# Optimization experiments

Hardware: AMD Instinct MI355X
Metric: run time of the kernel (lower is better)

The kernel has to match this reference:

```python
import jax, jax.numpy as jnp
import numpy as np

EMBED_DIM = 512
NUM_HEADS = 8
HEAD_DIM = EMBED_DIM // NUM_HEADS
N = 4096
E = 131072
EPS = 1e-5
NEG = -1e9


def layer_norm(x, g, b):
    mu = jnp.mean(x, axis=-1, keepdims=True)
    var = jnp.mean(jnp.square(x - mu), axis=-1, keepdims=True)
    return (x - mu) * jax.lax.rsqrt(var + EPS) * g + b


def setup_inputs() -> dict:
    key = jax.random.key(0)
    ks = jax.random.split(key, 12)
    D = EMBED_DIM
    s = 1.0 / np.sqrt(D)
    return {
        "x": jax.random.normal(ks[0], (N, D), jnp.float32),
        "edge_index": jax.random.randint(ks[1], (2, E), 0, N, jnp.int64),
        "edge_weight": jax.random.uniform(ks[2], (E,), jnp.float32),
        "Wqkv": jax.random.normal(ks[3], (3 * D, D), jnp.float32) * s,
        "bqkv": jnp.zeros((3 * D,), jnp.float32),
        "Wo": jax.random.normal(ks[4], (D, D), jnp.float32) * s,
        "bo": jnp.zeros((D,), jnp.float32),
        "W1": jax.random.normal(ks[5], (D, D), jnp.float32) * s,
        "b1": jnp.zeros((D,), jnp.float32),
        "g1": jnp.ones((D,), jnp.float32),
        "beta1": jnp.zeros((D,), jnp.float32),
        "g2": jnp.ones((D,), jnp.float32),
        "beta2": jnp.zeros((D,), jnp.float32),
    }


def reference(x, edge_index, edge_weight, Wqkv, bqkv, Wo, bo, W1, b1, g1, beta1, g2, beta2):
    n = x.shape[0]
    # dense NxN additive bias: -1e9 everywhere, 0 on diagonal, edge weights at (dst, src)
    src, dst = edge_index[0], edge_index[1]
    diag = jnp.arange(n)
    bias = jnp.full((n, n), NEG, dtype=x.dtype)
    bias = bias.at[diag, diag].set(0.0)
    bias = bias.at[dst, src].set(edge_weight.astype(x.dtype))

    # multi-head self-attention (torch nn.MultiheadAttention semantics)
    qkv = x @ Wqkv.T + bqkv                       # (N, 3D)
    q, k, v = jnp.split(qkv, 3, axis=-1)          # each (N, D)
    q = q.reshape(n, NUM_HEADS, HEAD_DIM).transpose(1, 0, 2)  # (H, N, hd)
    k = k.reshape(n, NUM_HEADS, HEAD_DIM).transpose(1, 0, 2)
    v = v.reshape(n, NUM_HEADS, HEAD_DIM).transpose(1, 0, 2)
    scores = jnp.einsum("hnd,hmd->hnm", q, k) / np.sqrt(HEAD_DIM)  # (H, N, N)
    scores = scores + bias[None, :, :]
    attn = jax.nn.softmax(scores, axis=-1)
    out = jnp.einsum("hnm,hmd->hnd", attn, v)     # (H, N, hd)
    out = out.transpose(1, 0, 2).reshape(n, EMBED_DIM)
    attn_out = out @ Wo.T + bo

    # residual + LN + FFN (single linear, no activation) + residual + LN
    h = layer_norm(x + attn_out, g1, beta1)
    h = layer_norm(h + (h @ W1.T + b1), g2, beta2)
    return h
```

## Files before the change

### kernel.cpp

```cpp
#include <hip/hip_runtime.h>

#define NNODES 4096
#define DIM 512
#define QKVD 1536
#define MAXE 96

typedef __bf16 bf16_t;
typedef bf16_t bf16x8 __attribute__((ext_vector_type(8)));
typedef bf16_t bf16x2 __attribute__((ext_vector_type(2)));
typedef float f32x4 __attribute__((ext_vector_type(4)));
typedef unsigned int uint;

__global__ __launch_bounds__(256) void cast_all_k(const float* __restrict__ x,
                                                  const float* __restrict__ wqkv,
                                                  const float* __restrict__ wo,
                                                  const float* __restrict__ w1,
                                                  bf16_t* __restrict__ xb,
                                                  bf16_t* __restrict__ wqkvb,
                                                  bf16_t* __restrict__ wob,
                                                  bf16_t* __restrict__ w1b,
                                                  uint* __restrict__ deg) {
  int i = blockIdx.x * 256 + threadIdx.x;
  if (blockIdx.x < 16) deg[i] = 0u;
  const float* src;
  bf16_t* dst;
  int off;
  if (i < 524288) { src = x; dst = xb; off = i; }
  else if (i < 720896) { src = wqkv; dst = wqkvb; off = i - 524288; }
  else if (i < 786432) { src = wo; dst = wob; off = i - 720896; }
  else { src = w1; dst = w1b; off = i - 786432; }
  float4 v = ((const float4*)src)[off];
  dst[4 * off + 0] = (bf16_t)v.x;
  dst[4 * off + 1] = (bf16_t)v.y;
  dst[4 * off + 2] = (bf16_t)v.z;
  dst[4 * off + 3] = (bf16_t)v.w;
}

__global__ __launch_bounds__(256) void qkv_fill_k(const bf16_t* __restrict__ A,
                                                  const bf16_t* __restrict__ B,
                                                  const float* __restrict__ bias,
                                                  bf16_t* __restrict__ Cout,
                                                  const int* __restrict__ ei,
                                                  uint* __restrict__ deg,
                                                  int* __restrict__ colv,
                                                  uint* __restrict__ eidv, int E) {
  __shared__ bf16_t As[128][40];
  __shared__ bf16_t Bs[128][40];
  const int bid = blockIdx.x;
  const int t = threadIdx.x;

  if (bid >= 384) {
    int e = (bid - 384) * 256 + t;
    if (e < E) {
      int src = ei[e] & (NNODES - 1);
      int dst = ei[E + e] & (NNODES - 1);
      uint pos = atomicAdd(&deg[dst], 1u);
      if (pos < MAXE) {
        colv[dst * MAXE + pos] = src;
        eidv[dst * MAXE + pos] = (uint)e + 1u;
      }
    }
    return;
  }

  const int lane = t & 63, w = t >> 6;
  const int wr = (w >> 1) * 64, wc = (w & 1) * 64;
  const int m0 = (bid / 12) * 128, n0 = (bid % 12) * 128;
  f32x4 acc[4][4] = {};
  const int r_ld = t >> 2;
  const int c_ld = (t & 3) * 8;

  for (int k0 = 0; k0 < 512; k0 += 32) {
#pragma unroll
    for (int seg = 0; seg < 2; ++seg) {
      int row = r_ld + seg * 64;
      *(int4*)&As[row][c_ld] = *(const int4*)(A + (long)(m0 + row) * 512 + k0 + c_ld);
      *(int4*)&Bs[row][c_ld] = *(const int4*)(B + (long)(n0 + row) * 512 + k0 + c_ld);
    }
    __syncthreads();
    bf16x8 af[4], bfr[4];
    const int kg = (lane >> 4) * 8;
#pragma unroll
    for (int i = 0; i < 4; ++i) {
      af[i] = *(const bf16x8*)&As[wr + i * 16 + (lane & 15)][kg];
      bfr[i] = *(const bf16x8*)&Bs[wc + i * 16 + (lane & 15)][kg];
    }
#pragma unroll
    for (int i = 0; i < 4; ++i)
#pragma unroll
      for (int j = 0; j < 4; ++j)
        acc[i][j] = __builtin_amdgcn_mfma_f32_16x16x32_bf16(af[i], bfr[j], acc[i][j], 0, 0, 0);
    __syncthreads();
  }

  const int cr = (lane >> 4) * 4;
  const int cc = lane & 15;
#pragma unroll
  for (int i = 0; i < 4; ++i) {
#pragma unroll
    for (int j = 0; j < 4; ++j) {
      int n = n0 + wc + j * 16 + cc;
      float bv = bias[n];
#pragma unroll
      for (int r = 0; r < 4; ++r) {
        int m = m0 + wr + i * 16 + cr + r;
        Cout[(long)m * QKVD + n] = (bf16_t)(acc[i][j][r] + bv);
      }
    }
  }
}

template <bool OUT_BF16>
__global__ __launch_bounds__(256) void gemm_bt(const bf16_t* __restrict__ A,
                                               const bf16_t* __restrict__ B,
                                               const float* __restrict__ bias,
                                               void* __restrict__ Cout,
                                               int M, int Nt, int K) {
  __shared__ bf16_t As[128][40];
  __shared__ bf16_t Bs[64][40];
  const int t = threadIdx.x;
  const int lane = t & 63, w = t >> 6;
  const int wr = (w >> 1) * 64, wc = (w & 1) * 32;
  const int m0 = blockIdx.y * 128, n0 = blockIdx.x * 64;
  f32x4 acc[4][2] = {};
  const int r_ld = t >> 2;
  const int c_ld = (t & 3) * 8;

  for (int k0 = 0; k0 < K; k0 += 32) {
    *(int4*)&As[r_ld][c_ld] = *(const int4*)(A + (long)(m0 + r_ld) * K + k0 + c_ld);
    *(int4*)&As[r_ld + 64][c_ld] = *(const int4*)(A + (long)(m0 + r_ld + 64) * K + k0 + c_ld);
    *(int4*)&Bs[r_ld][c_ld] = *(const int4*)(B + (long)(n0 + r_ld) * K + k0 + c_ld);
    __syncthreads();
    bf16x8 af[4], bfr[2];
    const int kg = (lane >> 4) * 8;
#pragma unroll
    for (int i = 0; i < 4; ++i)
      af[i] = *(const bf16x8*)&As[wr + i * 16 + (lane & 15)][kg];
#pragma unroll
    for (int j = 0; j < 2; ++j)
      bfr[j] = *(const bf16x8*)&Bs[wc + j * 16 + (lane & 15)][kg];
#pragma unroll
    for (int i = 0; i < 4; ++i)
#pragma unroll
      for (int j = 0; j < 2; ++j)
        acc[i][j] = __builtin_amdgcn_mfma_f32_16x16x32_bf16(af[i], bfr[j], acc[i][j], 0, 0, 0);
    __syncthreads();
  }

  const int cr = (lane >> 4) * 4;
  const int cc = lane & 15;
#pragma unroll
  for (int i = 0; i < 4; ++i) {
#pragma unroll
    for (int j = 0; j < 2; ++j) {
      int n = n0 + wc + j * 16 + cc;
      float bv = bias[n];
#pragma unroll
      for (int r = 0; r < 4; ++r) {
        int m = m0 + wr + i * 16 + cr + r;
        float vv = acc[i][j][r] + bv;
        if (OUT_BF16)
          ((bf16_t*)Cout)[(long)m * Nt + n] = (bf16_t)vv;
        else
          ((float*)Cout)[(long)m * Nt + n] = vv;
      }
    }
  }
}

__global__ __launch_bounds__(256) void attn_fused_k(const bf16_t* __restrict__ qkv,
                                                    const float* __restrict__ ew,
                                                    const uint* __restrict__ deg,
                                                    const int* __restrict__ colv,
                                                    const uint* __restrict__ eidv,
                                                    bf16_t* __restrict__ outb) {
  __shared__ float scs[8][MAXE + 1];
  __shared__ int srcs[MAXE + 1];
  __shared__ uint eids[MAXE + 1];
  __shared__ int vld[MAXE + 1];
  __shared__ float invs_s[8];
  __shared__ float vacc[4][DIM];

  const int i = blockIdx.x;
  const int t = threadIdx.x;
  const int lane = t & 63, w = t >> 6;

  uint dg = deg[i];
  int L = (dg < (uint)MAXE) ? (int)dg : MAXE;
  int n = L + 1;

  if (t < L) {
    srcs[t] = colv[i * MAXE + t];
    eids[t] = eidv[i * MAXE + t];
  }
  if (t == L) { srcs[L] = i; eids[L] = 0u; }
  __syncthreads();

  if (t < n) {
    int sj = srcs[t];
    uint my = eids[t];
    int ok = 1;
    for (int j = 0; j < n; ++j)
      ok &= !((srcs[j] == sj) & (eids[j] > my));
    vld[t] = ok;
  }
  __syncthreads();

  const bf16x8 qv = *(const bf16x8*)(qkv + (long)i * QKVD + lane * 8);
  {
    int e = w;
    for (; e + 4 < n; e += 8) {
      int sa = srcs[e], sb = srcs[e + 4];
      const bf16x8 ka = *(const bf16x8*)(qkv + (long)sa * QKVD + DIM + lane * 8);
      const bf16x8 kb = *(const bf16x8*)(qkv + (long)sb * QKVD + DIM + lane * 8);
      float s0 = 0.f, s1 = 0.f;
#pragma unroll
      for (int j = 0; j < 8; ++j) {
        s0 += (float)qv[j] * (float)ka[j];
        s1 += (float)qv[j] * (float)kb[j];
      }
      s0 += __shfl_xor(s0, 1); s1 += __shfl_xor(s1, 1);
      s0 += __shfl_xor(s0, 2); s1 += __shfl_xor(s1, 2);
      s0 += __shfl_xor(s0, 4); s1 += __shfl_xor(s1, 4);
      if ((lane & 7) == 0) {
        int h = lane >> 3;
        float b0 = (eids[e] == 0u) ? 0.f : ew[eids[e] - 1u];
        float b1 = (eids[e + 4] == 0u) ? 0.f : ew[eids[e + 4] - 1u];
        scs[h][e] = vld[e] ? (s0 * 0.125f + b0) : -1e30f;
        scs[h][e + 4] = vld[e + 4] ? (s1 * 0.125f + b1) : -1e30f;
      }
    }
    if (e < n) {
      int sa = srcs[e];
      const bf16x8 ka = *(const bf16x8*)(qkv + (long)sa * QKVD + DIM + lane * 8);
      float s0 = 0.f;
#pragma unroll
      for (int j = 0; j < 8; ++j) s0 += (float)qv[j] * (float)ka[j];
      s0 += __shfl_xor(s0, 1);
      s0 += __shfl_xor(s0, 2);
      s0 += __shfl_xor(s0, 4);
      if ((lane & 7) == 0) {
        int h = lane >> 3;
        float b0 = (eids[e] == 0u) ? 0.f : ew[eids[e] - 1u];
        scs[h][e] = vld[e] ? (s0 * 0.125f + b0) : -1e30f;
      }
    }
  }
  __syncthreads();

#pragma unroll
  for (int hh = 0; hh < 2; ++hh) {
    int h = w * 2 + hh;
    float m = -1e30f;
    for (int e = lane; e < n; e += 64) m = fmaxf(m, scs[h][e]);
#pragma unroll
    for (int o = 32; o > 0; o >>= 1) m = fmaxf(m, __shfl_xor(m, o));
    float ps = 0.f;
    for (int e = lane; e < n; e += 64) {
      float ev = __expf(scs[h][e] - m);
      scs[h][e] = ev;
      ps += ev;
    }
#pragma unroll
    for (int o = 32; o > 0; o >>= 1) ps += __shfl_xor(ps, o);
    if (lane == 0) invs_s[h] = 1.f / ps;
  }
  __syncthreads();

  const int hl = lane >> 3;
  float a8[8] = {0.f, 0.f, 0.f, 0.f, 0.f, 0.f, 0.f, 0.f};
  {
    int e = w;
    for (; e + 4 < n; e += 8) {
      const bf16x8 v0 = *(const bf16x8*)(qkv + (long)srcs[e] * QKVD + 2 * DIM + lane * 8);
      const bf16x8 v1 = *(const bf16x8*)(qkv + (long)srcs[e + 4] * QKVD + 2 * DIM + lane * 8);
      float p0 = scs[hl][e], p1 = scs[hl][e + 4];
#pragma unroll
      for (int j = 0; j < 8; ++j) a8[j] += p0 * (float)v0[j] + p1 * (float)v1[j];
    }
    if (e < n) {
      const bf16x8 v0 = *(const bf16x8*)(qkv + (long)srcs[e] * QKVD + 2 * DIM + lane * 8);
      float p0 = scs[hl][e];
#pragma unroll
      for (int j = 0; j < 8; ++j) a8[j] += p0 * (float)v0[j];
    }
  }
#pragma unroll
  for (int j = 0; j < 8; ++j) vacc[w][lane * 8 + j] = a8[j];
  __syncthreads();

  {
    const int d0 = 2 * t;
    const int h = t >> 5;
    const float inv = invs_s[h];
    float s0 = vacc[0][d0] + vacc[1][d0] + vacc[2][d0] + vacc[3][d0];
    float s1 = vacc[0][d0 + 1] + vacc[1][d0 + 1] + vacc[2][d0 + 1] + vacc[3][d0 + 1];
    bf16x2 o2;
    o2[0] = (bf16_t)(s0 * inv);
    o2[1] = (bf16_t)(s1 * inv);
    *(bf16x2*)(outb + (long)i * DIM + d0) = o2;
  }
}

__global__ __launch_bounds__(64) void ln_k(const float* __restrict__ a,
                                           const float* __restrict__ b,
                                           const float* __restrict__ g,
                                           const float* __restrict__ beta,
                                           float* __restrict__ of,
                                           bf16_t* __restrict__ ob) {
  const int row = blockIdx.x;
  const int l = threadIdx.x;
  const float* pa = a + (long)row * DIM;
  const float* pb = b + (long)row * DIM;
  float v[8];
  float s = 0.f;
#pragma unroll
  for (int j = 0; j < 8; ++j) {
    int d = l + j * 64;
    v[j] = pa[d] + pb[d];
    s += v[j];
  }
#pragma unroll
  for (int o = 32; o > 0; o >>= 1) s += __shfl_xor(s, o);
  float mu = s * (1.f / 512.f);
  float q = 0.f;
#pragma unroll
  for (int j = 0; j < 8; ++j) {
    float dd = v[j] - mu;
    q += dd * dd;
  }
#pragma unroll
  for (int o = 32; o > 0; o >>= 1) q += __shfl_xor(q, o);
  float inv = rsqrtf(q * (1.f / 512.f) + 1e-5f);
#pragma unroll
  for (int j = 0; j < 8; ++j) {
    int d = l + j * 64;
    float y = (v[j] - mu) * inv * g[d] + beta[d];
    of[(long)row * DIM + d] = y;
    if (ob) ob[(long)row * DIM + d] = (bf16_t)y;
  }
}

extern "C" void kernel_launch(void* const* d_in, const int* in_sizes, int n_in,
                              void* d_out, int out_size, void* d_ws, size_t ws_size,
                              hipStream_t stream) {
  const float* x = (const float*)d_in[0];
  const int* ei = (const int*)d_in[1];
  const float* ew = (const float*)d_in[2];
  const float* Wqkv = (const float*)d_in[3];
  const float* bqkv = (const float*)d_in[4];
  const float* Wo = (const float*)d_in[5];
  const float* bo = (const float*)d_in[6];
  const float* W1 = (const float*)d_in[7];
  const float* b1 = (const float*)d_in[8];
  const float* g1 = (const float*)d_in[9];
  const float* be1 = (const float*)d_in[10];
  const float* g2 = (const float*)d_in[11];
  const float* be2 = (const float*)d_in[12];
  float* out = (float*)d_out;
  const int E = in_sizes[1] / 2;

  char* ws = (char*)d_ws;
  bf16_t* qkvb = (bf16_t*)(ws + 0);
  bf16_t* xb = (bf16_t*)(ws + 12582912);
  bf16_t* Wqkvb = (bf16_t*)(ws + 16777216);
  bf16_t* Wob = (bf16_t*)(ws + 18350080);
  bf16_t* W1b = (bf16_t*)(ws + 18874368);
  bf16_t* outb = (bf16_t*)(ws + 19398656);
  float* h = (float*)(ws + 23592960);
  bf16_t* hb = (bf16_t*)(ws + 31981568);
  float* f = (float*)(ws + 36175872);
  uint* deg = (uint*)(ws + 23592960);
  int* colv = (int*)(ws + 23609344);
  uint* eidv = (uint*)(ws + 25182208);
  float* attn_out = (float*)(ws + 0);

  cast_all_k<<<3328, 256, 0, stream>>>(x, Wqkv, Wo, W1, xb, Wqkvb, Wob, W1b, deg);

  qkv_fill_k<<<384 + (E + 255) / 256, 256, 0, stream>>>(
      xb, Wqkvb, bqkv, qkvb, ei, deg, colv, eidv, E);

  attn_fused_k<<<NNODES, 256, 0, stream>>>(qkvb, ew, deg, colv, eidv, outb);

  gemm_bt<false><<<dim3(DIM / 64, NNODES / 128), 256, 0, stream>>>(
      outb, Wob, bo, (void*)attn_out, NNODES, DIM, DIM);

  ln_k<<<NNODES, 64, 0, stream>>>(x, attn_out, g1, be1, h, hb);

  gemm_bt<false><<<dim3(DIM / 64, NNODES / 128), 256, 0, stream>>>(
      hb, W1b, b1, (void*)f, NNODES, DIM, DIM);

  ln_k<<<NNODES, 64, 0, stream>>>(h, f, g2, be2, out, nullptr);
}
```

Measured before the change: 107.0 us.

## Fuse fp32-to-bf16 casts into QKV GEMM loads and unroll edge gathers wider

The standalone cast kernel is removed. The QKV GEMM now reads fp32 x and Wqkv directly and converts them to bf16 as it stages tiles into shared memory, and the Wo/W1 casts run as extra blocks inside the same launch. deg is zeroed with a hipMemsetAsync. The attention kernel's K-score and V-accumulate loops now process four edges per iteration instead of two, to expose more memory-level parallelism. In exchange, the GEMM reads twice as many bytes per tile (fp32) and x/Wqkv are reconverted for each tile that uses them.

Result: slower. 114.2 us (+6.7%).

```diff
diff --git a/kernel.cpp b/kernel.cpp
--- a/kernel.cpp
+++ b/kernel.cpp
@@ -11,54 +11,56 @@
 typedef float f32x4 __attribute__((ext_vector_type(4)));
 typedef unsigned int uint;
 
-__global__ __launch_bounds__(256) void cast_all_k(const float* __restrict__ x,
-                                                  const float* __restrict__ wqkv,
-                                                  const float* __restrict__ wo,
-                                                  const float* __restrict__ w1,
-                                                  bf16_t* __restrict__ xb,
-                                                  bf16_t* __restrict__ wqkvb,
-                                                  bf16_t* __restrict__ wob,
-                                                  bf16_t* __restrict__ w1b,
-                                                  uint* __restrict__ deg) {
-  int i = blockIdx.x * 256 + threadIdx.x;
-  if (blockIdx.x < 16) deg[i] = 0u;
-  const float* src;
-  bf16_t* dst;
-  int off;
-  if (i < 524288) { src = x; dst = xb; off = i; }
-  else if (i < 720896) { src = wqkv; dst = wqkvb; off = i - 524288; }
-  else if (i < 786432) { src = wo; dst = wob; off = i - 720896; }
-  else { src = w1; dst = w1b; off = i - 786432; }
-  float4 v = ((const float4*)src)[off];
-  dst[4 * off + 0] = (bf16_t)v.x;
-  dst[4 * off + 1] = (bf16_t)v.y;
-  dst[4 * off + 2] = (bf16_t)v.z;
-  dst[4 * off + 3] = (bf16_t)v.w;
-}
-
-__global__ __launch_bounds__(256) void qkv_fill_k(const bf16_t* __restrict__ A,
-                                                  const bf16_t* __restrict__ B,
-                                                  const float* __restrict__ bias,
-                                                  bf16_t* __restrict__ Cout,
-                                                  const int* __restrict__ ei,
-                                                  uint* __restrict__ deg,
-                                                  int* __restrict__ colv,
-                                                  uint* __restrict__ eidv, int E) {
+__device__ __forceinline__ bf16x8 cvt8(float4 a, float4 b) {
+  bf16x8 r;
+  r[0] = (bf16_t)a.x; r[1] = (bf16_t)a.y; r[2] = (bf16_t)a.z; r[3] = (bf16_t)a.w;
+  r[4] = (bf16_t)b.x; r[5] = (bf16_t)b.y; r[6] = (bf16_t)b.z; r[7] = (bf16_t)b.w;
+  return r;
+}
+
+__global__ __launch_bounds__(256) void qkv_fill_cast_k(const float* __restrict__ x,
+                                                       const float* __restrict__ wqkv,
+                                                       const float* __restrict__ bias,
+                                                       bf16_t* __restrict__ Cout,
+                                                       const int* __restrict__ ei,
+                                                       uint* __restrict__ deg,
+                                                       int* __restrict__ colv,
+                                                       uint* __restrict__ eidv, int E,
+                                                       const float* __restrict__ wo,
+                                                       const float* __restrict__ w1,
+                                                       bf16_t* __restrict__ wob,
+                                                       bf16_t* __restrict__ w1b) {
   __shared__ bf16_t As[128][40];
   __shared__ bf16_t Bs[128][40];
   const int bid = blockIdx.x;
   const int t = threadIdx.x;
+  const int fillB = (E + 255) / 256;
 
   if (bid >= 384) {
-    int e = (bid - 384) * 256 + t;
-    if (e < E) {
-      int src = ei[e] & (NNODES - 1);
-      int dst = ei[E + e] & (NNODES - 1);
-      uint pos = atomicAdd(&deg[dst], 1u);
-      if (pos < MAXE) {
-        colv[dst * MAXE + pos] = src;
-        eidv[dst * MAXE + pos] = (uint)e + 1u;
-      }
+    int r = bid - 384;
+    if (r < fillB) {
+      int e = r * 256 + t;
+      if (e < E) {
+        int src = ei[e] & (NNODES - 1);
+        int dst = ei[E + e] & (NNODES - 1);
+        uint pos = atomicAdd(&deg[dst], 1u);
+        if (pos < MAXE) {
+          colv[dst * MAXE + pos] = src;
+          eidv[dst * MAXE + pos] = (uint)e + 1u;
+        }
+      }
+    } else {
+      int i = (r - fillB) * 256 + t;
+      const float* src;
+      bf16_t* dst;
+      int off;
+      if (i < 65536) { src = wo; dst = wob; off = i; }
+      else { src = w1; dst = w1b; off = i - 65536; }
+      float4 v = ((const float4*)src)[off];
+      dst[4 * off + 0] = (bf16_t)v.x;
+      dst[4 * off + 1] = (bf16_t)v.y;
+      dst[4 * off + 2] = (bf16_t)v.z;
+      dst[4 * off + 3] = (bf16_t)v.w;
     }
     return;
   }
@@ -74,8 +76,14 @@
 #pragma unroll
     for (int seg = 0; seg < 2; ++seg) {
       int row = r_ld + seg * 64;
-      *(int4*)&As[row][c_ld] = *(const int4*)(A + (long)(m0 + row) * 512 + k0 + c_ld);
-      *(int4*)&Bs[row][c_ld] = *(const int4*)(B + (long)(n0 + row) * 512 + k0 + c_ld);
+      const float* ap = x + (long)(m0 + row) * 512 + k0 + c_ld;
+      const float* bp = wqkv + (long)(n0 + row) * 512 + k0 + c_ld;
+      float4 a0 = *(const float4*)ap;
+      float4 a1 = *(const float4*)(ap + 4);
+      float4 b0 = *(const float4*)bp;
+      float4 b1 = *(const float4*)(bp + 4);
+      *(bf16x8*)&As[row][c_ld] = cvt8(a0, a1);
+      *(bf16x8*)&Bs[row][c_ld] = cvt8(b0, b1);
     }
     __syncthreads();
     bf16x8 af[4], bfr[4];
@@ -209,40 +217,45 @@
   const bf16x8 qv = *(const bf16x8*)(qkv + (long)i * QKVD + lane * 8);
   {
     int e = w;
-    for (; e + 4 < n; e += 8) {
-      int sa = srcs[e], sb = srcs[e + 4];
-      const bf16x8 ka = *(const bf16x8*)(qkv + (long)sa * QKVD + DIM + lane * 8);
-      const bf16x8 kb = *(const bf16x8*)(qkv + (long)sb * QKVD + DIM + lane * 8);
-      float s0 = 0.f, s1 = 0.f;
+    for (; e + 12 < n; e += 16) {
+      const bf16x8 ka = *(const bf16x8*)(qkv + (long)srcs[e] * QKVD + DIM + lane * 8);
+      const bf16x8 kb = *(const bf16x8*)(qkv + (long)srcs[e + 4] * QKVD + DIM + lane * 8);
+      const bf16x8 kc = *(const bf16x8*)(qkv + (long)srcs[e + 8] * QKVD + DIM + lane * 8);
+      const bf16x8 kd = *(const bf16x8*)(qkv + (long)srcs[e + 12] * QKVD + DIM + lane * 8);
+      float d0 = 0.f, d1 = 0.f, d2 = 0.f, d3 = 0.f;
 #pragma unroll
       for (int j = 0; j < 8; ++j) {
-        s0 += (float)qv[j] * (float)ka[j];
-        s1 += (float)qv[j] * (float)kb[j];
-      }
-      s0 += __shfl_xor(s0, 1); s1 += __shfl_xor(s1, 1);
-      s0 += __shfl_xor(s0, 2); s1 += __shfl_xor(s1, 2);
-      s0 += __shfl_xor(s0, 4); s1 += __shfl_xor(s1, 4);
+        float q = (float)qv[j];
+        d0 += q * (float)ka[j];
+        d1 += q * (float)kb[j];
+        d2 += q * (float)kc[j];
+        d3 += q * (float)kd[j];
+      }
+#pragma unroll
+      for (int o = 1; o < 8; o <<= 1) {
+        d0 += __shfl_xor(d0, o);
+        d1 += __shfl_xor(d1, o);
+        d2 += __shfl_xor(d2, o);
+        d3 += __shfl_xor(d3, o);
+      }
       if ((lane & 7) == 0) {
         int h = lane >> 3;
-        float b0 = (eids[e] == 0u) ? 0.f : ew[eids[e] - 1u];
-        float b1 = (eids[e + 4] == 0u) ? 0.f : ew[eids[e + 4] - 1u];
-        scs[h][e] = vld[e] ? (s0 * 0.125f + b0) : -1e30f;
-        scs[h][e + 4] = vld[e + 4] ? (s1 * 0.125f + b1) : -1e30f;
-      }
-    }
-    if (e < n) {
-      int sa = srcs[e];
-      const bf16x8 ka = *(const bf16x8*)(qkv + (long)sa * QKVD + DIM + lane * 8);
-      float s0 = 0.f;
-#pragma unroll
-      for (int j = 0; j < 8; ++j) s0 += (float)qv[j] * (float)ka[j];
-      s0 += __shfl_xor(s0, 1);
-      s0 += __shfl_xor(s0, 2);
-      s0 += __shfl_xor(s0, 4);
+        scs[h][e] = vld[e] ? (d0 * 0.125f + ((eids[e] == 0u) ? 0.f : ew[eids[e] - 1u])) : -1e30f;
+        scs[h][e + 4] = vld[e + 4] ? (d1 * 0.125f + ((eids[e + 4] == 0u) ? 0.f : ew[eids[e + 4] - 1u])) : -1e30f;
+        scs[h][e + 8] = vld[e + 8] ? (d2 * 0.125f + ((eids[e + 8] == 0u) ? 0.f : ew[eids[e + 8] - 1u])) : -1e30f;
+        scs[h][e + 12] = vld[e + 12] ? (d3 * 0.125f + ((eids[e + 12] == 0u) ? 0.f : ew[eids[e + 12] - 1u])) : -1e30f;
+      }
+    }
+    for (; e < n; e += 4) {
+      const bf16x8 ka = *(const bf16x8*)(qkv + (long)srcs[e] * QKVD + DIM + lane * 8);
+      float d0 = 0.f;
+#pragma unroll
+      for (int j = 0; j < 8; ++j) d0 += (float)qv[j] * (float)ka[j];
+#pragma unroll
+      for (int o = 1; o < 8; o <<= 1) d0 += __shfl_xor(d0, o);
       if ((lane & 7) == 0) {
         int h = lane >> 3;
-        float b0 = (eids[e] == 0u) ? 0.f : ew[eids[e] - 1u];
-        scs[h][e] = vld[e] ? (s0 * 0.125f + b0) : -1e30f;
+        scs[h][e] = vld[e] ? (d0 * 0.125f + ((eids[e] == 0u) ? 0.f : ew[eids[e] - 1u])) : -1e30f;
       }
     }
   }
@@ -271,14 +284,17 @@
   float a8[8] = {0.f, 0.f, 0.f, 0.f, 0.f, 0.f, 0.f, 0.f};
   {
     int e = w;
-    for (; e + 4 < n; e += 8) {
+    for (; e + 12 < n; e += 16) {
       const bf16x8 v0 = *(const bf16x8*)(qkv + (long)srcs[e] * QKVD + 2 * DIM + lane * 8);
       const bf16x8 v1 = *(const bf16x8*)(qkv + (long)srcs[e + 4] * QKVD + 2 * DIM + lane * 8);
-      float p0 = scs[hl][e], p1 = scs[hl][e + 4];
-#pragma unroll
-      for (int j = 0; j < 8; ++j) a8[j] += p0 * (float)v0[j] + p1 * (float)v1[j];
-    }
-    if (e < n) {
+      const bf16x8 v2 = *(const bf16x8*)(qkv + (long)srcs[e + 8] * QKVD + 2 * DIM + lane * 8);
+      const bf16x8 v3 = *(const bf16x8*)(qkv + (long)srcs[e + 12] * QKVD + 2 * DIM + lane * 8);
+      float p0 = scs[hl][e], p1 = scs[hl][e + 4], p2 = scs[hl][e + 8], p3 = scs[hl][e + 12];
+#pragma unroll
+      for (int j = 0; j < 8; ++j)
+        a8[j] += p0 * (float)v0[j] + p1 * (float)v1[j] + p2 * (float)v2[j] + p3 * (float)v3[j];
+    }
+    for (; e < n; e += 4) {
       const bf16x8 v0 = *(const bf16x8*)(qkv + (long)srcs[e] * QKVD + 2 * DIM + lane * 8);
       float p0 = scs[hl][e];
 #pragma unroll
@@ -362,8 +378,6 @@
 
   char* ws = (char*)d_ws;
   bf16_t* qkvb = (bf16_t*)(ws + 0);
-  bf16_t* xb = (bf16_t*)(ws + 12582912);
-  bf16_t* Wqkvb = (bf16_t*)(ws + 16777216);
   bf16_t* Wob = (bf16_t*)(ws + 18350080);
   bf16_t* W1b = (bf16_t*)(ws + 18874368);
   bf16_t* outb = (bf16_t*)(ws + 19398656);
@@ -375,10 +389,11 @@
   uint* eidv = (uint*)(ws + 25182208);
   float* attn_out = (float*)(ws + 0);
 
-  cast_all_k<<<3328, 256, 0, stream>>>(x, Wqkv, Wo, W1, xb, Wqkvb, Wob, W1b, deg);
-
-  qkv_fill_k<<<384 + (E + 255) / 256, 256, 0, stream>>>(
-      xb, Wqkvb, bqkv, qkvb, ei, deg, colv, eidv, E);
+  hipMemsetAsync(deg, 0, 16384, stream);
+
+  const int fillB = (E + 255) / 256;
+  qkv_fill_cast_k<<<384 + fillB + 512, 256, 0, stream>>>(
+      x, Wqkv, bqkv, qkvb, ei, deg, colv, eidv, E, Wo, W1, Wob, W1b);
 
   attn_fused_k<<<NNODES, 256, 0, stream>>>(qkvb, ew, deg, colv, eidv, outb);
 
```
